# Optimization experiments

Hardware: AMD Instinct MI355X
Metric: run time of the kernel (lower is better)

## Reference

```python
import jax, jax.numpy as jnp
import numpy as np

FRAME_LEN = 400
HOP = 160
FFT_LEN = 512
PREEMPH = 0.97
MEL_FLOOR = 1.192092955078125e-07


def _hertz_to_mel(freq):
    return 1127.0 * np.log(1.0 + freq / 700.0)


def _mel_filter_bank(num_frequency_bins=256, num_mel_filters=80, min_frequency=20.0,
                     max_frequency=8000.0, sampling_rate=16000):
    mel_min = _hertz_to_mel(min_frequency)
    mel_max = _hertz_to_mel(max_frequency)
    mel_freqs = np.linspace(mel_min, mel_max, num_mel_filters + 2)
    # NOTE: source has filter_freqs = mel_freqs (mel-space, intentional replication of bug)
    filter_freqs = mel_freqs
    fft_bin_width = sampling_rate / (num_frequency_bins * 2)
    fft_freqs = _hertz_to_mel(fft_bin_width * np.arange(num_frequency_bins))
    filter_diff = np.diff(filter_freqs)
    slopes = filter_freqs[None, :] - fft_freqs[:, None]          # [256, 82]
    down_slopes = -slopes[:, :-2] / filter_diff[:-1]
    up_slopes = slopes[:, 2:] / filter_diff[1:]
    fb = np.maximum(0.0, np.minimum(down_slopes, up_slopes))      # [256, 80]
    # F.pad(mel_filters, (0,0,0,1)) -> one extra zero row -> [257, 80]
    return np.pad(fb, ((0, 1), (0, 0))).astype(np.float32)


def _window():
    n = np.arange(FRAME_LEN)
    hann = 0.5 - 0.5 * np.cos(2.0 * np.pi * n / (FRAME_LEN - 1))  # periodic=False
    return (hann ** 0.85).astype(np.float32)


def setup_inputs() -> dict:
    key = jax.random.key(0)
    T = 9_600_000  # 10 min @ 16 kHz
    raw_speech = jax.random.normal(key, (1, T), dtype=jnp.float32)
    return {
        "raw_speech": raw_speech,
        "mel_filters": jnp.asarray(_mel_filter_bank()),  # [257, 80]
        "window": jnp.asarray(_window()),                # [400]
    }


def reference(raw_speech, mel_filters, window):
    wav = raw_speech.reshape(-1) * 32768.0  # * 2**15
    num_frames = 1 + (wav.shape[0] - FRAME_LEN) // HOP
    idx = jnp.arange(num_frames)[:, None] * HOP + jnp.arange(FRAME_LEN)[None, :]
    frames = wav[idx]                                         # [F, 400]
    frames = frames - frames.mean(axis=1, keepdims=True)      # remove DC offset
    # preemphasis: y[0] = x[0]*(1-p), y[n] = x[n] - p*x[n-1]
    pre = jnp.concatenate(
        [frames[:, :1] * (1.0 - PREEMPH), frames[:, 1:] - PREEMPH * frames[:, :-1]],
        axis=1,
    )
    pre = pre * window
    padded = jnp.pad(pre, ((0, 0), (0, FFT_LEN - FRAME_LEN)))  # [F, 512]
    spec = jnp.abs(jnp.fft.rfft(padded, axis=1)) ** 2          # [F, 257]
    mel = jnp.log(jnp.maximum(spec @ mel_filters, MEL_FLOOR))  # [F, 80]
    mean = mel.mean(axis=0, keepdims=True)
    var = mel.var(axis=0, keepdims=True, ddof=1)               # unbiased
    return (mel - mean) / jnp.sqrt(var + 1e-7)
```

## Files before the change

### kernel.cpp

```cpp
#include <hip/hip_runtime.h>
#include <math.h>

#define FRAME_LEN 400
#define HOP 160
#define NMEL 80
#define PREEMPH 0.97f
#define MEL_FLOOR 1.192092955078125e-07f
#define PPW 4
#define NSHADOW 8

#ifndef __has_builtin
#define __has_builtin(x) 0
#endif
#if __has_builtin(__builtin_amdgcn_permlane16_swap) && __has_builtin(__builtin_amdgcn_permlane32_swap)
#define USE_PLSWAP 1
#else
#define USE_PLSWAP 0
#endif

__device__ __forceinline__ float2 cadd(float2 a, float2 b){ return make_float2(a.x+b.x, a.y+b.y); }
__device__ __forceinline__ float2 csub(float2 a, float2 b){ return make_float2(a.x-b.x, a.y-b.y); }
__device__ __forceinline__ float2 cmul(float2 a, float2 b){ return make_float2(a.x*b.x-a.y*b.y, a.x*b.y+a.y*b.x); }

__device__ __forceinline__ float bperm(int addr, float v) {
    return __int_as_float(__builtin_amdgcn_ds_bpermute(addr, __float_as_int(v)));
}
template<int C>
__device__ __forceinline__ float dppf(float v) {
    return __int_as_float(__builtin_amdgcn_update_dpp(0, __float_as_int(v), C, 0xF, 0xF, false));
}
__device__ __forceinline__ float wscan_add(float v) {
    v += __int_as_float(__builtin_amdgcn_update_dpp(0, __float_as_int(v), 0x111, 0xF, 0xF, false));
    v += __int_as_float(__builtin_amdgcn_update_dpp(0, __float_as_int(v), 0x112, 0xF, 0xF, false));
    v += __int_as_float(__builtin_amdgcn_update_dpp(0, __float_as_int(v), 0x114, 0xF, 0xF, false));
    v += __int_as_float(__builtin_amdgcn_update_dpp(0, __float_as_int(v), 0x118, 0xF, 0xF, false));
    v += __int_as_float(__builtin_amdgcn_update_dpp(0, __float_as_int(v), 0x142, 0xA, 0xF, false));
    v += __int_as_float(__builtin_amdgcn_update_dpp(0, __float_as_int(v), 0x143, 0xC, 0xF, false));
    return v;
}

#if USE_PLSWAP
typedef unsigned int uint2v __attribute__((ext_vector_type(2)));
__device__ __forceinline__ void bflytw16(float2& A, float2& B, float2 tw) {
    uint2v sx = __builtin_amdgcn_permlane16_swap(__float_as_uint(A.x), __float_as_uint(B.x), false, false);
    uint2v sy = __builtin_amdgcn_permlane16_swap(__float_as_uint(A.y), __float_as_uint(B.y), false, false);
    float lx = __uint_as_float(sx.x), hx = __uint_as_float(sx.y);
    float ly = __uint_as_float(sy.x), hy = __uint_as_float(sy.y);
    float cr = tw.x * hx - tw.y * hy;
    float ci = tw.x * hy + tw.y * hx;
    float r1x = lx + cr, r2x = lx - cr;
    float r1y = ly + ci, r2y = ly - ci;
    uint2v tx = __builtin_amdgcn_permlane16_swap(__float_as_uint(r1x), __float_as_uint(r2x), false, false);
    uint2v ty = __builtin_amdgcn_permlane16_swap(__float_as_uint(r1y), __float_as_uint(r2y), false, false);
    A = make_float2(__uint_as_float(tx.x), __uint_as_float(ty.x));
    B = make_float2(__uint_as_float(tx.y), __uint_as_float(ty.y));
}
__device__ __forceinline__ void bflytw32(float2& A, float2& B, float2 tw) {
    uint2v sx = __builtin_amdgcn_permlane32_swap(__float_as_uint(A.x), __float_as_uint(B.x), false, false);
    uint2v sy = __builtin_amdgcn_permlane32_swap(__float_as_uint(A.y), __float_as_uint(B.y), false, false);
    float lx = __uint_as_float(sx.x), hx = __uint_as_float(sx.y);
    float ly = __uint_as_float(sy.x), hy = __uint_as_float(sy.y);
    float cr = tw.x * hx - tw.y * hy;
    float ci = tw.x * hy + tw.y * hx;
    float r1x = lx + cr, r2x = lx - cr;
    float r1y = ly + ci, r2y = ly - ci;
    uint2v tx = __builtin_amdgcn_permlane32_swap(__float_as_uint(r1x), __float_as_uint(r2x), false, false);
    uint2v ty = __builtin_amdgcn_permlane32_swap(__float_as_uint(r1y), __float_as_uint(r2y), false, false);
    A = make_float2(__uint_as_float(tx.x), __uint_as_float(ty.x));
    B = make_float2(__uint_as_float(tx.y), __uint_as_float(ty.y));
}
#endif

__global__ __launch_bounds__(256) void setup_kernel(const float* __restrict__ window,
                                                    float* __restrict__ frtab,
                                                    int* __restrict__ kstab,
                                                    float* __restrict__ wftab,
                                                    float* __restrict__ twtab)
{
    const int bid = blockIdx.x;
    const int t = threadIdx.x;
    if (bid == 0) {
        __shared__ float uu[256];
        const double mel_min = 1127.0 * log(1.0 + 20.0 / 700.0);
        const double mel_max = 1127.0 * log(1.0 + 8000.0 / 700.0);
        const double dstep = (mel_max - mel_min) / 81.0;
        {
            double fhz = 31.25 * (double)t;
            double m = 1127.0 * log(1.0 + fhz / 700.0);
            uu[t] = (float)((m - mel_min) / dstep);
        }
        __syncthreads();
        {
            float u = uu[t];
            frtab[t] = u - floorf(u);
        }
        if (t < 82) {
            double fhz = 700.0 * (exp((mel_min + (double)t * dstep) / 1127.0) - 1.0);
            int k = (int)ceil(fhz / 31.25);
            k = max(0, min(256, k));
            while (k > 0 && uu[k - 1] >= (float)t) --k;
            while (k < 256 && uu[k] < (float)t) ++k;
            kstab[t] = k;
        }
        if (t < 64) {
            const int l = t;
            const int bl = __brev((unsigned)l) >> 26;
            float* o = twtab + 24 * l;
            #pragma unroll
            for (int j = 1; j <= 3; ++j) {
                int d = 1 << j;
                float2 tw = make_float2(1.f, 0.f);
                if (l & d) {
                    float tt = (float)(l & (d - 1));
                    float ang = -3.1415926535897932f * tt / (float)d;
                    sincosf(ang, &tw.y, &tw.x);
                }
                o[2 * (j - 1)]     = tw.x;
                o[2 * (j - 1) + 1] = tw.y;
            }
            {
                float a16 = -3.1415926535897932f * (float)(l & 15) * (1.0f / 16.0f);
                float a32 = -3.1415926535897932f * (float)(l & 31) * (1.0f / 32.0f);
                float s16, c16, s32, c32;
                sincosf(a16, &s16, &c16);
                sincosf(a32, &s32, &c32);
                o[6] = c16; o[7] = s16; o[8] = c32; o[9] = s32;
            }
            #pragma unroll
            for (int q = 1; q < 4; ++q) {
                float ang = -6.283185307179586f * (float)(bl * q) * (1.0f / 256.0f);
                float sv, cv;
                sincosf(ang, &sv, &cv);
                o[8 + 2 * q] = cv; o[9 + 2 * q] = sv;
            }
            #pragma unroll
            for (int q = 0; q < 4; ++q) {
                int k = 4 * l + q;
                float ang = -3.1415926535897932f * (float)k * (1.0f / 256.0f);
                float sv, cv;
                sincosf(ang, &sv, &cv);
                o[16 + 2 * q] = cv; o[17 + 2 * q] = sv;
            }
        }
    } else {
        if (t >= 64) return;
        const int k = bid - 1;
        float sr = 0.f, si = 0.f;
        #pragma unroll
        for (int j = 0; j < 7; ++j) {
            int n = t + 64 * j;
            if (n < FRAME_LEN) {
                float wv = window[n] * 32768.f;
                int m = (k * n) & 511;
                float ang = -3.1415926535897932f * (float)m * (1.0f / 256.0f);
                float sv, cv;
                sincosf(ang, &sv, &cv);
                sr = fmaf(wv, cv, sr);
                si = fmaf(wv, sv, si);
            }
        }
        sr = wscan_add(sr);
        si = wscan_add(si);
        if (t == 63) { wftab[2 * k] = sr; wftab[2 * k + 1] = si; }
    }
}

__global__ __launch_bounds__(64, 8) void feat_kernel(
    const float* __restrict__ raw, const float* __restrict__ window,
    float* __restrict__ mel_out, double* __restrict__ accum,
    const float* __restrict__ frtab, const int* __restrict__ kstab,
    const float* __restrict__ wftab, const float* __restrict__ twtab, int F)
{
    __shared__ __align__(16) float wlds[FRAME_LEN];
    __shared__ __align__(16) float xu[560];
    __shared__ __align__(16) float pfx[2][256];

    const int l = threadIdx.x;

    for (int i = l; i < FRAME_LEN; i += 64) wlds[i] = window[i] * 32768.f;

    const int bl   = __brev((unsigned)l) >> 26;
    const int adrX = (l ^ 63) << 2;
    const int adr0 = ((64 - l) & 63) << 2;

    float sg[4];
    #pragma unroll
    for (int j = 0; j < 4; ++j) sg[j] = (l & (1 << j)) ? -1.f : 1.f;

    float2 dt[3], tw16, tw32, w2[4], wk[4];
    {
        const float2* tl = (const float2*)(twtab + 24 * l);
        dt[0] = tl[0];
        dt[1] = tl[1];
        dt[2] = tl[2];
        tw16  = tl[3];
        tw32  = tl[4];
        w2[1] = tl[5];
        w2[2] = tl[6];
        w2[3] = tl[7];
        wk[0] = tl[8];
        wk[1] = tl[9];
        wk[2] = tl[10];
        wk[3] = tl[11];
    }
#if !USE_PLSWAP
    float2 dtf[2];
    float sgf[2];
    #pragma unroll
    for (int j = 4; j <= 5; ++j) {
        int d = 1 << j;
        sgf[j - 4] = (l & d) ? -1.f : 1.f;
        float2 tw = make_float2(1.f, 0.f);
        if (l & d) {
            float tt = (float)(l & (d - 1));
            float ang = -3.1415926535897932f * tt / (float)d;
            sincosf(ang, &tw.y, &tw.x);
        }
        dtf[j - 4] = tw;
    }
#endif

    float wfr[4], wfi[4];
    {
        const float2* wf2 = (const float2*)wftab;
        float2 w0 = wf2[4 * l], w1 = wf2[4 * l + 1], w2v = wf2[4 * l + 2], w3 = wf2[4 * l + 3];
        wfr[0] = w0.x; wfi[0] = w0.y; wfr[1] = w1.x; wfi[1] = w1.y;
        wfr[2] = w2v.x; wfi[2] = w2v.y; wfr[3] = w3.x; wfi[3] = w3.y;
    }

    float fr1[4];
    {
        float4 fv = *(const float4*)(frtab + 4 * l);
        fr1[0] = fv.x; fr1[1] = fv.y; fr1[2] = fv.z; fr1[3] = fv.w;
    }
    int a0 = kstab[l], b0 = kstab[l + 1], e0 = kstab[l + 2];
    int a1 = 1, b1 = 1, e1 = 1;
    if (l < 16) { a1 = kstab[64 + l]; b1 = kstab[65 + l]; e1 = kstab[66 + l]; }

    const int NP = (F + 1) >> 1;
    const int basePair = blockIdx.x * PPW;

    float acc_s0 = 0.f, acc_q0 = 0.f;
    float acc_s1 = 0.f, acc_q1 = 0.f;

    for (int fi = 0; fi < PPW; ++fi) {
        int P = basePair + fi;
        if (P >= NP) break;
        int fA = 2 * P;
        bool hasB = (fA + 1) < F;

        const float4* g4 = (const float4*)(raw + (size_t)fA * HOP);
        float4 a = g4[l];
        float4 b = make_float4(0.f, 0.f, 0.f, 0.f);
        float4 c = make_float4(0.f, 0.f, 0.f, 0.f);
        if (hasB || l < 36) b = g4[64 + l];
        if (hasB && l < 12) c = g4[128 + l];
        ((float4*)xu)[l] = a;
        ((float4*)xu)[64 + l] = b;
        if (l < 12) ((float4*)xu)[128 + l] = c;

        float as = a.x + a.y + a.z + a.w;
        float bs = b.x + b.y + b.z + b.w;
        float cs = c.x + c.y + c.z + c.w;
        float sA8 = as + (l < 36 ? bs : 0.f);
        float sB8 = (l >= 40 ? as : 0.f) + bs + cs;
        float totA = __int_as_float(__builtin_amdgcn_readlane(__float_as_int(wscan_add(sA8)), 63));
        float totB = __int_as_float(__builtin_amdgcn_readlane(__float_as_int(wscan_add(sB8)), 63));
        float KA = totA * (1.0f / (float)FRAME_LEN) * (1.0f - PREEMPH);
        float KB = totB * (1.0f / (float)FRAME_LEN) * (1.0f - PREEMPH);

        float2 Z[2][4];
        #pragma unroll
        for (int r = 0; r < 4; ++r) {
            int off = 128 * r + 2 * bl;
            if (off < FRAME_LEN) {
                float2 xA = *(const float2*)(xu + off);
                float2 xB = *(const float2*)(xu + 160 + off);
                float xm1A = (off == 0) ? xA.x : xu[off - 1];
                float xm1B = (off == 0) ? xB.x : xu[159 + off];
                float2 wn  = *(const float2*)(wlds + off);
                Z[0][r] = make_float2(fmaf(-PREEMPH, xm1A, xA.x) * wn.x,
                                      fmaf(-PREEMPH, xA.x,  xA.y) * wn.y);
                Z[1][r] = make_float2(fmaf(-PREEMPH, xm1B, xB.x) * wn.x,
                                      fmaf(-PREEMPH, xB.x,  xB.y) * wn.y);
            } else {
                Z[0][r] = make_float2(0.f, 0.f);
                Z[1][r] = make_float2(0.f, 0.f);
            }
        }

        #pragma unroll
        for (int s = 0; s < 2; ++s) {
            float2 t0 = cadd(Z[s][0], Z[s][2]);
            float2 t1 = csub(Z[s][0], Z[s][2]);
            float2 t2 = cadd(Z[s][1], Z[s][3]);
            float2 t3 = csub(Z[s][1], Z[s][3]);
            Z[s][0] = cadd(t0, t2);
            Z[s][2] = csub(t0, t2);
            Z[s][1] = make_float2(t1.x + t3.y, t1.y - t3.x);
            Z[s][3] = make_float2(t1.x - t3.y, t1.y + t3.x);
            #pragma unroll
            for (int q = 1; q < 4; ++q) Z[s][q] = cmul(Z[s][q], w2[q]);
        }

        #pragma unroll
        for (int s = 0; s < 2; ++s)
        #pragma unroll
        for (int q = 0; q < 4; ++q) {
            float ox = dppf<0xB1>(Z[s][q].x), oy = dppf<0xB1>(Z[s][q].y);
            Z[s][q].x = fmaf(sg[0], Z[s][q].x, ox);
            Z[s][q].y = fmaf(sg[0], Z[s][q].y, oy);
        }
        #pragma unroll
        for (int s = 0; s < 2; ++s)
        #pragma unroll
        for (int q = 0; q < 4; ++q) {
            float2 Zw = cmul(Z[s][q], dt[0]);
            float ox = dppf<0x4E>(Zw.x), oy = dppf<0x4E>(Zw.y);
            Z[s][q].x = fmaf(sg[1], Zw.x, ox);
            Z[s][q].y = fmaf(sg[1], Zw.y, oy);
        }
        #pragma unroll
        for (int s = 0; s < 2; ++s)
        #pragma unroll
        for (int q = 0; q < 4; ++q) {
            float2 Zw = cmul(Z[s][q], dt[1]);
            float ox = __shfl_xor(Zw.x, 4, 64), oy = __shfl_xor(Zw.y, 4, 64);
            Z[s][q].x = fmaf(sg[2], Zw.x, ox);
            Z[s][q].y = fmaf(sg[2], Zw.y, oy);
        }
        #pragma unroll
        for (int s = 0; s < 2; ++s)
        #pragma unroll
        for (int q = 0; q < 4; ++q) {
            float2 Zw = cmul(Z[s][q], dt[2]);
            float ox = dppf<0x128>(Zw.x), oy = dppf<0x128>(Zw.y);
            Z[s][q].x = fmaf(sg[3], Zw.x, ox);
            Z[s][q].y = fmaf(sg[3], Zw.y, oy);
        }
#if USE_PLSWAP
        #pragma unroll
        for (int s = 0; s < 2; ++s) {
            bflytw16(Z[s][0], Z[s][1], tw16);
            bflytw16(Z[s][2], Z[s][3], tw16);
        }
        #pragma unroll
        for (int s = 0; s < 2; ++s) {
            bflytw32(Z[s][0], Z[s][1], tw32);
            bflytw32(Z[s][2], Z[s][3], tw32);
        }
#else
        #pragma unroll
        for (int s = 0; s < 2; ++s)
        #pragma unroll
        for (int q = 0; q < 4; ++q) {
            float2 Zw = cmul(Z[s][q], dtf[0]);
            float ox = __shfl_xor(Zw.x, 16, 64), oy = __shfl_xor(Zw.y, 16, 64);
            Z[s][q].x = fmaf(sgf[0], Zw.x, ox);
            Z[s][q].y = fmaf(sgf[0], Zw.y, oy);
        }
        #pragma unroll
        for (int s = 0; s < 2; ++s)
        #pragma unroll
        for (int q = 0; q < 4; ++q) {
            float2 Zw = cmul(Z[s][q], dtf[1]);
            float ox = __shfl_xor(Zw.x, 32, 64), oy = __shfl_xor(Zw.y, 32, 64);
            Z[s][q].x = fmaf(sgf[1], Zw.x, ox);
            Z[s][q].y = fmaf(sgf[1], Zw.y, oy);
        }
#endif

        #pragma unroll
        for (int s = 0; s < 2; ++s) {
            float Ks = (s == 0) ? KA : KB;
            float zcr[4], zci[4];
            zcr[0] = bperm(adr0, Z[s][0].x);
            zci[0] = bperm(adr0, Z[s][0].y);
            zcr[1] = bperm(adrX, Z[s][3].x);
            zci[1] = bperm(adrX, Z[s][3].y);
            zcr[2] = bperm(adrX, Z[s][2].x);
            zci[2] = bperm(adrX, Z[s][2].y);
            zcr[3] = bperm(adrX, Z[s][1].x);
            zci[3] = bperm(adrX, Z[s][1].y);

            float pw[4], pv[4];
            #pragma unroll
            for (int q = 0; q < 4; ++q) {
                float Er = 0.5f * (Z[s][q].x + zcr[q]);
                float Ei = 0.5f * (Z[s][q].y - zci[q]);
                float Or = 0.5f * (Z[s][q].y + zci[q]);
                float Oi = 0.5f * (zcr[q] - Z[s][q].x);
                float Xr = Er + Or * wk[q].x - Oi * wk[q].y;
                float Xi = Ei + Or * wk[q].y + Oi * wk[q].x;
                Xr = fmaf(-Ks, wfr[q], Xr);
                Xi = fmaf(-Ks, wfi[q], Xi);
                pw[q] = Xr * Xr + Xi * Xi;
                pv[q] = pw[q] * fr1[q];
            }
            float A0 = pw[0], A1 = A0 + pw[1], A2 = A1 + pw[2], A3 = A2 + pw[3];
            float B0 = pv[0], B1 = B0 + pv[1], B2 = B1 + pv[2], B3 = B2 + pv[3];
            float sA = wscan_add(A3);
            float sB = wscan_add(B3);
            float exA = sA - A3;
            float exB = sB - B3;
            float* pP = pfx[0];
            float* pF = pfx[1];
            ((float4*)pP)[l] = make_float4(exA + A0, exA + A1, exA + A2, exA + A3);
            ((float4*)pF)[l] = make_float4(exB + B0, exB + B1, exB + B2, exB + B3);

            int f = fA + s;
            bool act = (s == 0) || hasB;
            if (act) {
                float E1a = pF[a0 - 1], E1b = pF[b0 - 1], E1e = pF[e0 - 1];
                float EAb = pP[b0 - 1], EAe = pP[e0 - 1];
                float acc = fmaf(2.f, E1b, -E1a) - E1e + (EAe - EAb);
                float v = __logf(fmaxf(acc, MEL_FLOOR));
                mel_out[(size_t)f * NMEL + l] = v;
                acc_s0 += v; acc_q0 = fmaf(v, v, acc_q0);
                if (l < 16) {
                    float F1a = pF[a1 - 1], F1b = pF[b1 - 1], F1e = pF[e1 - 1];
                    float FAb = pP[b1 - 1], FAe = pP[e1 - 1];
                    float ac2 = fmaf(2.f, F1b, -F1a) - F1e + (FAe - FAb);
                    float v1 = __logf(fmaxf(ac2, MEL_FLOOR));
                    mel_out[(size_t)f * NMEL + 64 + l] = v1;
                    acc_s1 += v1; acc_q1 = fmaf(v1, v1, acc_q1);
                }
            }
        }
    }

    double* A = accum + (blockIdx.x & (NSHADOW - 1)) * 160;
    atomicAdd(&A[l], (double)acc_s0);
    atomicAdd(&A[80 + l], (double)acc_q0);
    if (l < 16) {
        atomicAdd(&A[64 + l], (double)acc_s1);
        atomicAdd(&A[144 + l], (double)acc_q1);
    }
}

__global__ __launch_bounds__(256) void norm_kernel(
    float* __restrict__ mel, const double* __restrict__ accum, int F)
{
    __shared__ float s_mean[NMEL], s_inv[NMEL];
    int t = threadIdx.x;
    if (t < NMEL) {
        double S = 0.0, Q = 0.0;
        #pragma unroll
        for (int j = 0; j < NSHADOW; ++j) {
            S += accum[j * 160 + t];
            Q += accum[j * 160 + 80 + t];
        }
        double mean = S / (double)F;
        double var = (Q - S * S / (double)F) / (double)(F - 1);
        s_mean[t] = (float)mean;
        s_inv[t]  = (float)(1.0 / sqrt(var + 1e-7));
    }
    __syncthreads();
    unsigned n = (unsigned)F * NMEL;
    unsigned stride = gridDim.x * 256u * 4u;
    unsigned i = (blockIdx.x * 256u + (unsigned)t) * 4u;
    int c = (int)(i % NMEL);
    float m0 = s_mean[c],     r0 = s_inv[c];
    float m1 = s_mean[c + 1], r1 = s_inv[c + 1];
    float m2 = s_mean[c + 2], r2 = s_inv[c + 2];
    float m3 = s_mean[c + 3], r3 = s_inv[c + 3];
    for (; i < n; i += stride) {
        float4 v = *(float4*)(mel + i);
        v.x = (v.x - m0) * r0;
        v.y = (v.y - m1) * r1;
        v.z = (v.z - m2) * r2;
        v.w = (v.w - m3) * r3;
        *(float4*)(mel + i) = v;
    }
}

extern "C" void kernel_launch(void* const* d_in, const int* in_sizes, int n_in,
                              void* d_out, int out_size, void* d_ws, size_t ws_size,
                              hipStream_t stream)
{
    const float* raw = (const float*)d_in[0];
    const float* window = (const float*)d_in[2];
    float* out = (float*)d_out;

    int N = in_sizes[0];
    int F = 1 + (N - FRAME_LEN) / HOP;

    double* accum = (double*)d_ws;
    float*  frtab = (float*)((char*)d_ws + NSHADOW * 160 * sizeof(double));
    int*    kstab = (int*)((char*)d_ws + 11264);
    float*  wftab = (float*)((char*)d_ws + 11776);
    float*  twtab = (float*)((char*)d_ws + 13824);

    hipMemsetAsync(d_ws, 0, NSHADOW * 160 * sizeof(double), stream);
    setup_kernel<<<257, 256, 0, stream>>>(window, frtab, kstab, wftab, twtab);
    int NP = (F + 1) / 2;
    int gridA = (NP + PPW - 1) / PPW;
    feat_kernel<<<gridA, 64, 0, stream>>>(raw, window, out, accum, frtab, kstab, wftab, twtab, F);
    norm_kernel<<<2560, 256, 0, stream>>>(out, accum, F);
}
```

Baseline: 144.2 us.

## Double-buffer frame loads via global_load_lds prefetch of next frame pair

Doubles the LDS frame buffer and prefetches the next frame pair's raw samples while the current pair is processed. Where the builtin exists it uses direct global-to-LDS loads, so the data skips registers. The frame-sum computation moves to read from LDS during the preemphasis pass. This is meant to hide global load latency, at the cost of extra LDS per block, which may reduce occupancy. There is no barrier beyond a vmcnt wait, which relies on single-wave block semantics.

```diff
diff --git a/kernel.cpp b/kernel.cpp
--- a/kernel.cpp
+++ b/kernel.cpp
@@ -16,6 +16,15 @@
 #define USE_PLSWAP 1
 #else
 #define USE_PLSWAP 0
+#endif
+#if __has_builtin(__builtin_amdgcn_global_load_lds)
+#define USE_GLL 1
+typedef __attribute__((address_space(3))) void* as3_void_ptr;
+typedef const __attribute__((address_space(1))) void* as1_void_cptr;
+#define GLOAD_LDS(gsrc, ldst) \
+    __builtin_amdgcn_global_load_lds((as1_void_cptr)(gsrc), (as3_void_ptr)(ldst), 16, 0, 0)
+#else
+#define USE_GLL 0
 #endif
 
 __device__ __forceinline__ float2 cadd(float2 a, float2 b){ return make_float2(a.x+b.x, a.y+b.y); }
@@ -172,7 +181,7 @@
     const float* __restrict__ wftab, const float* __restrict__ twtab, int F)
 {
     __shared__ __align__(16) float wlds[FRAME_LEN];
-    __shared__ __align__(16) float xu[560];
+    __shared__ __align__(16) float xu[2][560];
     __shared__ __align__(16) float pfx[2][256];
 
     const int l = threadIdx.x;
@@ -243,42 +252,71 @@
     float acc_s0 = 0.f, acc_q0 = 0.f;
     float acc_s1 = 0.f, acc_q1 = 0.f;
 
+    if (basePair < NP) {
+        int fA0 = 2 * basePair;
+        bool hasB0 = (fA0 + 1) < F;
+        const float* g = raw + (size_t)fA0 * HOP;
+#if USE_GLL
+        GLOAD_LDS(g + 4 * l, xu[0]);
+        if (hasB0 || l < 36) GLOAD_LDS(g + 256 + 4 * l, xu[0] + 256);
+        if (hasB0 && l < 12) GLOAD_LDS(g + 512 + 4 * l, xu[0] + 512);
+#else
+        float4 a = ((const float4*)g)[l];
+        float4 b = make_float4(0.f,0.f,0.f,0.f);
+        float4 c = make_float4(0.f,0.f,0.f,0.f);
+        if (hasB0 || l < 36) b = ((const float4*)g)[64 + l];
+        if (hasB0 && l < 12) c = ((const float4*)g)[128 + l];
+        ((float4*)xu[0])[l] = a;
+        ((float4*)xu[0])[64 + l] = b;
+        if (l < 12) ((float4*)xu[0])[128 + l] = c;
+#endif
+    }
+
     for (int fi = 0; fi < PPW; ++fi) {
         int P = basePair + fi;
         if (P >= NP) break;
         int fA = 2 * P;
         bool hasB = (fA + 1) < F;
-
-        const float4* g4 = (const float4*)(raw + (size_t)fA * HOP);
-        float4 a = g4[l];
-        float4 b = make_float4(0.f, 0.f, 0.f, 0.f);
-        float4 c = make_float4(0.f, 0.f, 0.f, 0.f);
-        if (hasB || l < 36) b = g4[64 + l];
-        if (hasB && l < 12) c = g4[128 + l];
-        ((float4*)xu)[l] = a;
-        ((float4*)xu)[64 + l] = b;
-        if (l < 12) ((float4*)xu)[128 + l] = c;
-
-        float as = a.x + a.y + a.z + a.w;
-        float bs = b.x + b.y + b.z + b.w;
-        float cs = c.x + c.y + c.z + c.w;
-        float sA8 = as + (l < 36 ? bs : 0.f);
-        float sB8 = (l >= 40 ? as : 0.f) + bs + cs;
-        float totA = __int_as_float(__builtin_amdgcn_readlane(__float_as_int(wscan_add(sA8)), 63));
-        float totB = __int_as_float(__builtin_amdgcn_readlane(__float_as_int(wscan_add(sB8)), 63));
-        float KA = totA * (1.0f / (float)FRAME_LEN) * (1.0f - PREEMPH);
-        float KB = totB * (1.0f / (float)FRAME_LEN) * (1.0f - PREEMPH);
-
+        const int cur = fi & 1;
+
+        asm volatile("s_waitcnt vmcnt(0)" ::: "memory");
+
+        const bool ldn = (fi + 1 < PPW) && (P + 1 < NP);
+        if (ldn) {
+            int fAn = 2 * (P + 1);
+            bool hasBn = (fAn + 1) < F;
+            const float* g = raw + (size_t)fAn * HOP;
+            float* xn = xu[cur ^ 1];
+#if USE_GLL
+            GLOAD_LDS(g + 4 * l, xn);
+            if (hasBn || l < 36) GLOAD_LDS(g + 256 + 4 * l, xn + 256);
+            if (hasBn && l < 12) GLOAD_LDS(g + 512 + 4 * l, xn + 512);
+#else
+            float4 a = ((const float4*)g)[l];
+            float4 b = make_float4(0.f,0.f,0.f,0.f);
+            float4 c = make_float4(0.f,0.f,0.f,0.f);
+            if (hasBn || l < 36) b = ((const float4*)g)[64 + l];
+            if (hasBn && l < 12) c = ((const float4*)g)[128 + l];
+            ((float4*)xn)[l] = a;
+            ((float4*)xn)[64 + l] = b;
+            if (l < 12) ((float4*)xn)[128 + l] = c;
+#endif
+        }
+
+        const float* xc = xu[cur];
         float2 Z[2][4];
+        float smA = 0.f, smB = 0.f;
         #pragma unroll
         for (int r = 0; r < 4; ++r) {
             int off = 128 * r + 2 * bl;
             if (off < FRAME_LEN) {
-                float2 xA = *(const float2*)(xu + off);
-                float2 xB = *(const float2*)(xu + 160 + off);
-                float xm1A = (off == 0) ? xA.x : xu[off - 1];
-                float xm1B = (off == 0) ? xB.x : xu[159 + off];
+                float2 xA = *(const float2*)(xc + off);
+                float2 xB = *(const float2*)(xc + 160 + off);
+                float xm1A = (off == 0) ? xA.x : xc[off - 1];
+                float xm1B = (off == 0) ? xB.x : xc[159 + off];
                 float2 wn  = *(const float2*)(wlds + off);
+                smA += xA.x + xA.y;
+                smB += xB.x + xB.y;
                 Z[0][r] = make_float2(fmaf(-PREEMPH, xm1A, xA.x) * wn.x,
                                       fmaf(-PREEMPH, xA.x,  xA.y) * wn.y);
                 Z[1][r] = make_float2(fmaf(-PREEMPH, xm1B, xB.x) * wn.x,
@@ -288,6 +326,10 @@
                 Z[1][r] = make_float2(0.f, 0.f);
             }
         }
+        float totA = __int_as_float(__builtin_amdgcn_readlane(__float_as_int(wscan_add(smA)), 63));
+        float totB = __int_as_float(__builtin_amdgcn_readlane(__float_as_int(wscan_add(smB)), 63));
+        float KA = totA * (1.0f / (float)FRAME_LEN) * (1.0f - PREEMPH);
+        float KB = totB * (1.0f / (float)FRAME_LEN) * (1.0f - PREEMPH);
 
         #pragma unroll
         for (int s = 0; s < 2; ++s) {
```

Measured after the change: 142.3 us. Within noise of the previous version (-1.3%).
